# Performance work log

Measured on AMD Instinct MI355X. Metric: run time of the kernel, lower is better.

## Reference

```python
import jax, jax.numpy as jnp
import numpy as np

N = 100000   # nodes
E = 1600000  # edges
F = 128      # input/hidden dim
C = 3        # classes
G = 64       # graphs in batch


def setup_inputs() -> dict:
    key = jax.random.key(0)
    ks = jax.random.split(key, 12)
    s = 1.0 / np.sqrt(F)
    return {
        "x": jax.random.normal(ks[0], (N, F), dtype=jnp.float32),
        "edge_index": jax.random.randint(ks[1], (2, E), 0, N, dtype=jnp.int64),
        "batch": jnp.sort(jax.random.randint(ks[2], (N,), 0, G, dtype=jnp.int64)),
        "W1": jax.random.normal(ks[3], (F, F), dtype=jnp.float32) * s,
        "b1": jnp.zeros((F,), dtype=jnp.float32),
        "W2": jax.random.normal(ks[4], (F, F), dtype=jnp.float32) * s,
        "b2": jnp.zeros((F,), dtype=jnp.float32),
        "W3": jax.random.normal(ks[5], (F, F), dtype=jnp.float32) * s,
        "b3": jnp.zeros((F,), dtype=jnp.float32),
        "Wc": jax.random.normal(ks[6], (F, C), dtype=jnp.float32) * s,
        "bc": jnp.zeros((C,), dtype=jnp.float32),
    }


def reference(x, edge_index, batch, W1, b1, W2, b2, W3, b3, Wc, bc):
    n = x.shape[0]
    src, dst = edge_index[0], edge_index[1]
    # GCN adds self-loops: A_hat = A + I
    loops = jnp.arange(n, dtype=src.dtype)
    src_a = jnp.concatenate([src, loops])
    dst_a = jnp.concatenate([dst, loops])
    # symmetric normalization D^-1/2 (A+I) D^-1/2 (in-degree incl. self-loop)
    deg = jax.ops.segment_sum(jnp.ones_like(dst_a, dtype=x.dtype), dst_a, num_segments=n)
    dis = jnp.where(deg > 0, jax.lax.rsqrt(deg), 0.0)
    norm = dis[src_a] * dis[dst_a]  # [E+N]

    def gcn_conv(h, W, b):
        h = h @ W                                    # [N, F']
        msg = h[src_a] * norm[:, None]               # gather + scale
        agg = jax.ops.segment_sum(msg, dst_a, num_segments=n)  # scatter-add
        return agg + b

    h = jax.nn.relu(gcn_conv(x, W1, b1))   # dropout = identity in eval mode
    h = jax.nn.relu(gcn_conv(h, W2, b2))
    h = jax.nn.relu(gcn_conv(h, W3, b3))

    # global_mean_pool over graph ids
    sums = jax.ops.segment_sum(h, batch, num_segments=G)
    cnt = jax.ops.segment_sum(jnp.ones((n,), dtype=h.dtype), batch, num_segments=G)
    pooled = sums / jnp.maximum(cnt, 1.0)[:, None]
    return pooled @ Wc + bc
```

## Files before the change

### kernel.cpp

```cpp
#include <hip/hip_runtime.h>
#include <cstdint>
#include <cstddef>

#define FDIM 128
#define CHUNK 4096
#define BSHIFT 8
#define BMASK 255
#define MAXB 512

typedef unsigned short ushort_t;
typedef __attribute__((ext_vector_type(8))) short short8;
typedef __attribute__((ext_vector_type(4))) float floatx4;

__device__ inline ushort_t f2bf(float f) {
  unsigned u = __float_as_uint(f);
  u += 0x7fffu + ((u >> 16) & 1u);
  return (ushort_t)(u >> 16);
}
__device__ inline float bf2f(ushort_t h) {
  return __uint_as_float((unsigned)h << 16);
}

__global__ __launch_bounds__(256) void k_histw(const int* __restrict__ dst, int e,
                                               int nb, int* __restrict__ chunkHist,
                                               int nch,
                                               const float* __restrict__ W1,
                                               const float* __restrict__ W2,
                                               const float* __restrict__ W3,
                                               ushort_t* __restrict__ wsw,
                                               int* __restrict__ counter,
                                               float* __restrict__ partials_g,
                                               int g_count) {
  if (blockIdx.x >= (unsigned)nch) {
    int b = blockIdx.x - nch;
    if (b == 3) {
      for (int i = threadIdx.x; i < g_count * FDIM; i += 256) partials_g[i] = 0.f;
      return;
    }
    if (b == 0 && threadIdx.x == 0) *counter = 0;
    const float* W = (b == 0) ? W1 : (b == 1) ? W2 : W3;
    ushort_t* o = wsw + (size_t)b * 16384;
    for (int idx = threadIdx.x; idx < 16384; idx += 256) {
      int j = idx & 7;
      int lane = (idx >> 3) & 63;
      int ct = (idx >> 9) & 7;
      int kc = idx >> 12;
      int k = kc * 32 + (lane >> 4) * 8 + j;
      int col = (lane & 15) * 8 + ct;
      o[idx] = f2bf(W[k * FDIM + col]);
    }
    return;
  }
  __shared__ int h[MAXB];
  int c = blockIdx.x;
  int base = c * CHUNK;
  int end = min(base + CHUNK, e);
  for (int i = threadIdx.x; i < nb; i += 256) h[i] = 0;
  __syncthreads();
  for (int i = base + threadIdx.x; i < end; i += 256)
    atomicAdd(&h[dst[i] >> BSHIFT], 1);
  __syncthreads();
  for (int b = threadIdx.x; b < nb; b += 256)
    chunkHist[(size_t)c * nb + b] = h[b];
}

__global__ __launch_bounds__(512) void k_scan1(const int* __restrict__ chunkHist,
                                               int nchunks, int nb,
                                               int* __restrict__ chunkOff,
                                               int* __restrict__ bucketTotal,
                                               int* __restrict__ bucketBase,
                                               int* __restrict__ counter) {
  __shared__ int sb[512];
  int b = blockIdx.x;
  int t = threadIdx.x;
  int base = 0;
  for (int c0 = 0; c0 < nchunks; c0 += 512) {
    int c = c0 + t;
    int v = (c < nchunks) ? chunkHist[(size_t)c * nb + b] : 0;
    int x = v;
    sb[t] = x;
    __syncthreads();
    for (int off = 1; off < 512; off <<= 1) {
      int y = (t >= off) ? sb[t - off] : 0;
      __syncthreads();
      x += y;
      sb[t] = x;
      __syncthreads();
    }
    if (c < nchunks) chunkOff[(size_t)c * nb + b] = base + x - v;
    int tileTot = sb[511];
    __syncthreads();
    base += tileTot;
  }
  if (t == 0) {
    bucketTotal[b] = base;
    bucketBase[b] = atomicAdd(counter, base);
  }
}

__global__ __launch_bounds__(256) void k_bin(const int* __restrict__ src,
                                             const int* __restrict__ dst, int e, int nb,
                                             const int* __restrict__ chunkHist,
                                             const int* __restrict__ chunkOff,
                                             const int* __restrict__ bucketBase,
                                             unsigned* __restrict__ binned) {
  __shared__ unsigned sortedL[CHUNK];
  __shared__ int gtarget[CHUNK];
  __shared__ int lbase[MAXB], lcur[MAXB], gbase[MAXB];
  __shared__ int stmp[256];
  int c = blockIdx.x;
  int base = c * CHUNK;
  int end = min(base + CHUNK, e);
  for (int i = threadIdx.x; i < nb; i += 256) {
    lbase[i] = chunkHist[(size_t)c * nb + i];
    gbase[i] = bucketBase[i] + chunkOff[(size_t)c * nb + i];
  }
  __syncthreads();
  int carry = 0;
  for (int i0 = 0; i0 < nb; i0 += 256) {
    int i = i0 + threadIdx.x;
    int v = (i < nb) ? lbase[i] : 0;
    int x = v;
    stmp[threadIdx.x] = x;
    __syncthreads();
    for (int off = 1; off < 256; off <<= 1) {
      int y = (threadIdx.x >= off) ? stmp[threadIdx.x - off] : 0;
      __syncthreads();
      x += y;
      stmp[threadIdx.x] = x;
      __syncthreads();
    }
    if (i < nb) lbase[i] = carry + x - v;
    int tileTot = stmp[255];
    __syncthreads();
    carry += tileTot;
  }
  for (int i = threadIdx.x; i < nb; i += 256) lcur[i] = lbase[i];
  __syncthreads();
  for (int i = base + threadIdx.x; i < end; i += 256) {
    int d = dst[i];
    int sv = src[i];
    int b = d >> BSHIFT;
    int slot = atomicAdd(&lcur[b], 1);
    sortedL[slot] = ((unsigned)sv << BSHIFT) | (unsigned)(d & BMASK);
    gtarget[slot] = gbase[b] + (slot - lbase[b]);
  }
  __syncthreads();
  for (int i = threadIdx.x; i < end - base; i += 256)
    binned[gtarget[i]] = sortedL[i];
}

__global__ __launch_bounds__(256) void k_fill2(const unsigned* __restrict__ binned,
                                               const int* __restrict__ bucketBase,
                                               const int* __restrict__ bucketTotal,
                                               int n,
                                               int* __restrict__ rowStart,
                                               int* __restrict__ deg,
                                               float* __restrict__ dis,
                                               unsigned* __restrict__ colPacked) {
  __shared__ int h[256], sb[256], cur[256];
  int b = blockIdx.x;
  int s0 = bucketBase[b], s1 = s0 + bucketTotal[b];
  int nodeBase = b << BSHIFT;
  int t = threadIdx.x;
  h[t] = 0;
  __syncthreads();
  for (int i = s0 + t; i < s1; i += 256) atomicAdd(&h[binned[i] & BMASK], 1);
  __syncthreads();
  int v = h[t];
  int x = v;
  sb[t] = x;
  __syncthreads();
  for (int off = 1; off < 256; off <<= 1) {
    int y = (t >= off) ? sb[t - off] : 0;
    __syncthreads();
    x += y;
    sb[t] = x;
    __syncthreads();
  }
  int start = s0 + x - v;
  cur[t] = start;
  int node = nodeBase + t;
  if (node < n) {
    rowStart[node] = start;
    deg[node] = v;
    dis[node] = rsqrtf((float)(v + 1));
  }
  __syncthreads();
  for (int i = s0 + t; i < s1; i += 256) {
    unsigned en = binned[i];
    int slot = atomicAdd(&cur[en & BMASK], 1);
    colPacked[slot] = en >> BSHIFT;
  }
}

template <int INBF, int EDGW>
__global__ __launch_bounds__(256) void k_mm(const void* __restrict__ Ain,
                                            const ushort_t* __restrict__ Wsw,
                                            ushort_t* __restrict__ O, int n, int mmb,
                                            unsigned* __restrict__ colPacked, int e,
                                            const float* __restrict__ dis) {
  if (EDGW && blockIdx.x >= (unsigned)mmb) {
    int base = (blockIdx.x - mmb) * 2048 + threadIdx.x;
    for (int k = 0; k < 8; ++k) {
      int i = base + k * 256;
      if (i < e) {
        unsigned p = colPacked[i];
        colPacked[i] = p | ((unsigned)f2bf(dis[p]) << 17);
      }
    }
    return;
  }
  __shared__ ushort_t Bs[16384];
  int tid = threadIdx.x;
  for (int q = tid; q < 2048; q += 256)
    ((uint4*)Bs)[q] = ((const uint4*)Wsw)[q];
  __syncthreads();

  int w = tid >> 6;
  int lane = tid & 63;
  int quad = lane >> 4;
  int l15 = lane & 15;
  int rb = blockIdx.x * 128 + w * 32;
  const float* Af = (const float*)Ain;
  const ushort_t* Ab = (const ushort_t*)Ain;

  int row0 = rb + l15;
  int row1 = rb + 16 + l15;
  bool v0 = row0 < n, v1 = row1 < n;

  floatx4 acc[2][8];
#pragma unroll
  for (int rt = 0; rt < 2; ++rt)
#pragma unroll
    for (int ct = 0; ct < 8; ++ct) acc[rt][ct] = floatx4{0.f, 0.f, 0.f, 0.f};

#pragma unroll
  for (int kc = 0; kc < 4; ++kc) {
    int k0 = kc * 32 + quad * 8;
    short8 a0 = short8{0, 0, 0, 0, 0, 0, 0, 0};
    short8 a1 = short8{0, 0, 0, 0, 0, 0, 0, 0};
    if (INBF) {
      if (v0) a0 = *(const short8*)&Ab[(size_t)row0 * FDIM + k0];
      if (v1) a1 = *(const short8*)&Ab[(size_t)row1 * FDIM + k0];
    } else {
      if (v0) {
        float4 f0 = *(const float4*)&Af[(size_t)row0 * FDIM + k0];
        float4 f1 = *(const float4*)&Af[(size_t)row0 * FDIM + k0 + 4];
        a0 = short8{(short)f2bf(f0.x), (short)f2bf(f0.y), (short)f2bf(f0.z),
                    (short)f2bf(f0.w), (short)f2bf(f1.x), (short)f2bf(f1.y),
                    (short)f2bf(f1.z), (short)f2bf(f1.w)};
      }
      if (v1) {
        float4 f0 = *(const float4*)&Af[(size_t)row1 * FDIM + k0];
        float4 f1 = *(const float4*)&Af[(size_t)row1 * FDIM + k0 + 4];
        a1 = short8{(short)f2bf(f0.x), (short)f2bf(f0.y), (short)f2bf(f0.z),
                    (short)f2bf(f0.w), (short)f2bf(f1.x), (short)f2bf(f1.y),
                    (short)f2bf(f1.z), (short)f2bf(f1.w)};
      }
    }
#pragma unroll
    for (int ct = 0; ct < 8; ++ct) {
      short8 bf = *(const short8*)&Bs[((kc * 8 + ct) * 64 + lane) * 8];
      acc[0][ct] = __builtin_amdgcn_mfma_f32_16x16x32_bf16(a0, bf, acc[0][ct], 0, 0, 0);
      acc[1][ct] = __builtin_amdgcn_mfma_f32_16x16x32_bf16(a1, bf, acc[1][ct], 0, 0, 0);
    }
  }

#pragma unroll
  for (int rt = 0; rt < 2; ++rt) {
#pragma unroll
    for (int i = 0; i < 4; ++i) {
      int row = rb + rt * 16 + quad * 4 + i;
      if (row < n) {
        uint4 pk;
        pk.x = (unsigned)f2bf(acc[rt][0][i]) | ((unsigned)f2bf(acc[rt][1][i]) << 16);
        pk.y = (unsigned)f2bf(acc[rt][2][i]) | ((unsigned)f2bf(acc[rt][3][i]) << 16);
        pk.z = (unsigned)f2bf(acc[rt][4][i]) | ((unsigned)f2bf(acc[rt][5][i]) << 16);
        pk.w = (unsigned)f2bf(acc[rt][6][i]) | ((unsigned)f2bf(acc[rt][7][i]) << 16);
        *(uint4*)&O[(size_t)row * FDIM + l15 * 8] = pk;
      }
    }
  }
}

template <int POOL>
__global__ __launch_bounds__(256) void k_agg(const ushort_t* __restrict__ Hin,
                                             ushort_t* __restrict__ Hout,
                                             const int* __restrict__ rowStart,
                                             const int* __restrict__ degE,
                                             const unsigned* __restrict__ colPacked,
                                             const float* __restrict__ dis,
                                             const float* __restrict__ bias, int n,
                                             const int* __restrict__ batch,
                                             float* __restrict__ partials_blk,
                                             float* __restrict__ partials_g) {
  __shared__ float pool_s[POOL ? 4 * FDIM : 4];
  __shared__ int done;
  int tid = threadIdx.x;
  if (POOL) {
    if (tid == 0) done = 0;
    __syncthreads();
  }
  int node = blockIdx.x * 8 + (tid >> 5);
  int lane = tid & 31;
  bool act = node < n;
  if (!POOL && !act) return;
  float a0 = 0.f, a1 = 0.f, a2 = 0.f, a3 = 0.f;
  if (act) {
    const uint2* hin = (const uint2*)Hin;
    float di = dis[node];
    uint2 su = hin[(size_t)node * 32 + lane];
    float ws = di * di;
    a0 = ws * __uint_as_float(su.x << 16);
    a1 = ws * __uint_as_float(su.x & 0xffff0000u);
    a2 = ws * __uint_as_float(su.y << 16);
    a3 = ws * __uint_as_float(su.y & 0xffff0000u);
    int s0 = rowStart[node], cnt = degE[node];
    const unsigned* __restrict__ cp = colPacked + s0;

    int j = 0;
    int main8 = cnt & ~7;
    if (main8) {
      unsigned pv[8];
#pragma unroll
      for (int k = 0; k < 8; ++k) pv[k] = cp[k];
      for (;;) {
        uint2 u[8];
#pragma unroll
        for (int k = 0; k < 8; ++k)
          u[k] = hin[(size_t)(pv[k] & 0x1ffffu) * 32 + lane];
        int jn = j + 8;
        bool more = jn < main8;
        unsigned pn[8];
        if (more) {
#pragma unroll
          for (int k = 0; k < 8; ++k) pn[k] = cp[jn + k];
        }
#pragma unroll
        for (int k = 0; k < 8; ++k) {
          float w = di * __uint_as_float((pv[k] >> 17) << 16);
          a0 += w * __uint_as_float(u[k].x << 16);
          a1 += w * __uint_as_float(u[k].x & 0xffff0000u);
          a2 += w * __uint_as_float(u[k].y << 16);
          a3 += w * __uint_as_float(u[k].y & 0xffff0000u);
        }
        j = jn;
        if (!more) break;
#pragma unroll
        for (int k = 0; k < 8; ++k) pv[k] = pn[k];
      }
    }
    if (j + 4 <= cnt) {
      unsigned pv[4];
#pragma unroll
      for (int k = 0; k < 4; ++k) pv[k] = cp[j + k];
      uint2 u[4];
#pragma unroll
      for (int k = 0; k < 4; ++k)
        u[k] = hin[(size_t)(pv[k] & 0x1ffffu) * 32 + lane];
#pragma unroll
      for (int k = 0; k < 4; ++k) {
        float w = di * __uint_as_float((pv[k] >> 17) << 16);
        a0 += w * __uint_as_float(u[k].x << 16);
        a1 += w * __uint_as_float(u[k].x & 0xffff0000u);
        a2 += w * __uint_as_float(u[k].y << 16);
        a3 += w * __uint_as_float(u[k].y & 0xffff0000u);
      }
      j += 4;
    }
    for (; j < cnt; ++j) {
      unsigned pv = cp[j];
      int sidx = (int)(pv & 0x1ffffu);
      float w = di * __uint_as_float((pv >> 17) << 16);
      uint2 u = hin[(size_t)sidx * 32 + lane];
      a0 += w * __uint_as_float(u.x << 16);
      a1 += w * __uint_as_float(u.x & 0xffff0000u);
      a2 += w * __uint_as_float(u.y << 16);
      a3 += w * __uint_as_float(u.y & 0xffff0000u);
    }
    float4 b = ((const float4*)bias)[lane];
    a0 = fmaxf(a0 + b.x, 0.f);
    a1 = fmaxf(a1 + b.y, 0.f);
    a2 = fmaxf(a2 + b.z, 0.f);
    a3 = fmaxf(a3 + b.w, 0.f);
    if (!POOL) {
      uint2 o;
      o.x = (unsigned)f2bf(a0) | ((unsigned)f2bf(a1) << 16);
      o.y = (unsigned)f2bf(a2) | ((unsigned)f2bf(a3) << 16);
      ((uint2*)Hout)[(size_t)node * 32 + lane] = o;
    }
  }
  if (POOL) {
    int base = blockIdx.x * 8;
    int lastn = min(base + 7, n - 1);
    int g0 = batch[base];
    int sg = (g0 == batch[lastn]) ? g0 : -1;
    int w = tid >> 6;
    int wl = tid & 63;
    int pl = wl ^ 32;
    float p0 = __shfl(a0, pl);
    float p1 = __shfl(a1, pl);
    float p2 = __shfl(a2, pl);
    float p3 = __shfl(a3, pl);
    if (sg >= 0) {
      if (wl < 32) {
        float4 v = {a0 + p0, a1 + p1, a2 + p2, a3 + p3};
        *(float4*)&pool_s[w * FDIM + wl * 4] = v;
      }
    } else {
      if (wl < 32) *(float4*)&pool_s[w * FDIM + wl * 4] = float4{0.f, 0.f, 0.f, 0.f};
      if (act) {
        int gn = batch[node];
        float* pg = &partials_g[(size_t)gn * FDIM + lane * 4];
        atomicAdd(pg + 0, a0);
        atomicAdd(pg + 1, a1);
        atomicAdd(pg + 2, a2);
        atomicAdd(pg + 3, a3);
      }
    }
    __threadfence_block();
    int old = 0;
    if (wl == 0) old = atomicAdd(&done, 1);
    old = __shfl(old, 0);
    if (old == 3) {
      int c = wl * 2;
      float s0 = 0.f, s1 = 0.f;
#pragma unroll
      for (int ww = 0; ww < 4; ++ww) {
        float2 v = *(float2*)&pool_s[ww * FDIM + c];
        s0 += v.x;
        s1 += v.y;
      }
      *(float2*)&partials_blk[(size_t)blockIdx.x * FDIM + c] = float2{s0, s1};
    }
  }
}


__device__ inline int lower_bound_batch(const int* __restrict__ batch, int n, int g) {
  int lo = 0, hi = n;
  while (lo < hi) {
    int mid = (lo + hi) >> 1;
    if (batch[mid] < g) lo = mid + 1;
    else hi = mid;
  }
  return lo;
}

__global__ __launch_bounds__(128) void k_final(const float* __restrict__ partials_blk,
                                               const float* __restrict__ partials_g,
                                               const int* __restrict__ batch, int n,
                                               const float* __restrict__ Wc,
                                               const float* __restrict__ bc,
                                               float* __restrict__ out, int g_count) {
  __shared__ int se[2];
  __shared__ float red[6];
  int t = threadIdx.x;
  int g = blockIdx.x;
  if (t < 2) se[t] = lower_bound_batch(batch, n, g + t);
  __syncthreads();
  int s = se[0], e = se[1];
  float acc = partials_g[(size_t)g * FDIM + t];
  for (int b = (s + 7) >> 3; b * 8 < e; ++b) {
    if (b * 8 + 8 <= e || e >= n)
      acc += partials_blk[(size_t)b * FDIM + t];
  }
  float inv = 1.0f / (float)max(e - s, 1);
  float sv = acc * inv;
#pragma unroll
  for (int c = 0; c < 3; ++c) {
    float v = sv * Wc[t * 3 + c];
#pragma unroll
    for (int off = 1; off < 64; off <<= 1) v += __shfl_xor(v, off);
    if ((t & 63) == 0) red[(t >> 6) * 3 + c] = v;
  }
  __syncthreads();
  if (t < 3) out[g * 3 + t] = red[t] + red[3 + t] + bc[t];
}


extern "C" void kernel_launch(void* const* d_in, const int* in_sizes, int n_in,
                              void* d_out, int out_size, void* d_ws, size_t ws_size,
                              hipStream_t stream) {
  const float* x = (const float*)d_in[0];
  const int* edge = (const int*)d_in[1];
  const int* batch = (const int*)d_in[2];
  const float* W1 = (const float*)d_in[3];
  const float* b1 = (const float*)d_in[4];
  const float* W2 = (const float*)d_in[5];
  const float* b2 = (const float*)d_in[6];
  const float* W3 = (const float*)d_in[7];
  const float* b3 = (const float*)d_in[8];
  const float* Wc = (const float*)d_in[9];
  const float* bc = (const float*)d_in[10];
  float* out = (float*)d_out;

  const int N = in_sizes[0] / FDIM;
  const int E = in_sizes[1] / 2;
  const int G = out_size / 3;
  const int* src = edge;
  const int* dst = edge + E;

  const int NCH = (E + CHUNK - 1) / CHUNK;
  const int NB = (N + (1 << BSHIFT) - 1) >> BSHIFT;

  char* ws = (char*)d_ws;
  size_t off = 0;
  auto carve = [&](size_t bytes) -> void* {
    void* p = ws + off;
    off = (off + bytes + 255) & ~(size_t)255;
    return p;
  };
  int aggb = (N + 7) / 8;
  ushort_t* h0 = (ushort_t*)carve((size_t)N * FDIM * 2);
  ushort_t* h1 = (ushort_t*)carve((size_t)N * FDIM * 2);
  unsigned* colPacked = (unsigned*)carve((size_t)E * 4);
  unsigned* binned = (unsigned*)carve((size_t)E * 4);
  int* chunkHist = (int*)carve((size_t)NCH * NB * 4);
  int* chunkOff = (int*)carve((size_t)NCH * NB * 4);
  int* bucketTotal = (int*)carve((size_t)NB * 4);
  int* bucketBase = (int*)carve((size_t)NB * 4);
  int* counter = (int*)carve(256);
  int* rowStart = (int*)carve((size_t)N * 4);
  int* deg = (int*)carve((size_t)N * 4);
  float* dis = (float*)carve((size_t)N * 4);
  float* partials_g = (float*)carve((size_t)G * FDIM * 4);
  float* partials_blk = (float*)carve((size_t)aggb * FDIM * 4);
  ushort_t* wsw = (ushort_t*)carve((size_t)3 * 16384 * 2);
  (void)n_in;
  (void)ws_size;

  k_histw<<<NCH + 4, 256, 0, stream>>>(dst, E, NB, chunkHist, NCH, W1, W2, W3, wsw,
                                       counter, partials_g, G);
  k_scan1<<<NB, 512, 0, stream>>>(chunkHist, NCH, NB, chunkOff, bucketTotal,
                                  bucketBase, counter);
  k_bin<<<NCH, 256, 0, stream>>>(src, dst, E, NB, chunkHist, chunkOff, bucketBase,
                                 binned);
  k_fill2<<<NB, 256, 0, stream>>>(binned, bucketBase, bucketTotal, N, rowStart, deg,
                                  dis, colPacked);

  int mmb = (N + 127) / 128;
  int ewb = (E + 2047) / 2048;
  k_mm<0, 1><<<mmb + ewb, 256, 0, stream>>>(x, wsw, h0, N, mmb, colPacked, E, dis);
  k_agg<0><<<aggb, 256, 0, stream>>>(h0, h1, rowStart, deg, colPacked, dis, b1, N,
                                     nullptr, nullptr, nullptr);
  k_mm<1, 0><<<mmb, 256, 0, stream>>>(h1, wsw + 16384, h0, N, mmb, nullptr, 0,
                                      nullptr);
  k_agg<0><<<aggb, 256, 0, stream>>>(h0, h1, rowStart, deg, colPacked, dis, b2, N,
                                     nullptr, nullptr, nullptr);
  k_mm<1, 0><<<mmb, 256, 0, stream>>>(h1, wsw + 32768, h0, N, mmb, nullptr, 0,
                                      nullptr);
  k_agg<1><<<aggb, 256, 0, stream>>>(h0, h1, rowStart, deg, colPacked, dis, b3, N,
                                     batch, partials_blk, partials_g);

  k_final<<<G, 128, 0, stream>>>(partials_blk, partials_g, batch, N, Wc, bc, out, G);
}
```

Measured before the change: 434.7 us.

## Fuse first matmul into histogram kernel and drop packed edge weights

Moves the layer-1 matmul (x@W1, converting W1 to bf16 in-block) into the front kernel alongside the dst histogram and W2/W3 swizzle, so it runs concurrently with CSR construction instead of after it. Removes the edge-weight packing pass that embedded bf16 dis into colPacked; aggregation now gathers dis[src] directly per edge, adding an extra scattered 4-byte load per edge in each of three layers. Also widens k_final to 512 threads, splitting the per-graph partial-block reduction across 4 row groups.

```diff
diff --git a/kernel.cpp b/kernel.cpp
--- a/kernel.cpp
+++ b/kernel.cpp
@@ -21,26 +21,41 @@
   return __uint_as_float((unsigned)h << 16);
 }
 
-__global__ __launch_bounds__(256) void k_histw(const int* __restrict__ dst, int e,
-                                               int nb, int* __restrict__ chunkHist,
-                                               int nch,
-                                               const float* __restrict__ W1,
-                                               const float* __restrict__ W2,
-                                               const float* __restrict__ W3,
-                                               ushort_t* __restrict__ wsw,
-                                               int* __restrict__ counter,
-                                               float* __restrict__ partials_g,
-                                               int g_count) {
-  if (blockIdx.x >= (unsigned)nch) {
-    int b = blockIdx.x - nch;
-    if (b == 3) {
-      for (int i = threadIdx.x; i < g_count * FDIM; i += 256) partials_g[i] = 0.f;
+__global__ __launch_bounds__(256) void k_front(
+    const float* __restrict__ x, const float* __restrict__ W1,
+    const float* __restrict__ W2, const float* __restrict__ W3,
+    ushort_t* __restrict__ h0, int n, int mmb,
+    const int* __restrict__ dst, int e, int nb,
+    int* __restrict__ chunkHist, int nch,
+    ushort_t* __restrict__ wsw, int* __restrict__ counter,
+    float* __restrict__ partials_g, int g_count) {
+  __shared__ ushort_t Bs[16384];
+  int tid = threadIdx.x;
+  int bid = blockIdx.x;
+  if (bid >= mmb) {
+    int r = bid - mmb;
+    if (r < nch) {
+      int* h = (int*)Bs;
+      int base = r * CHUNK;
+      int end = min(base + CHUNK, e);
+      for (int i = tid; i < nb; i += 256) h[i] = 0;
+      __syncthreads();
+      for (int i = base + tid; i < end; i += 256)
+        atomicAdd(&h[dst[i] >> BSHIFT], 1);
+      __syncthreads();
+      for (int b = tid; b < nb; b += 256)
+        chunkHist[(size_t)r * nb + b] = h[b];
       return;
     }
-    if (b == 0 && threadIdx.x == 0) *counter = 0;
-    const float* W = (b == 0) ? W1 : (b == 1) ? W2 : W3;
+    int b = r - nch;
+    if (b == 2) {
+      for (int i = tid; i < g_count * FDIM; i += 256) partials_g[i] = 0.f;
+      return;
+    }
+    if (b == 0 && tid == 0) *counter = 0;
+    const float* W = (b == 0) ? W2 : W3;
     ushort_t* o = wsw + (size_t)b * 16384;
-    for (int idx = threadIdx.x; idx < 16384; idx += 256) {
+    for (int idx = tid; idx < 16384; idx += 256) {
       int j = idx & 7;
       int lane = (idx >> 3) & 63;
       int ct = (idx >> 9) & 7;
@@ -51,17 +66,85 @@
     }
     return;
   }
-  __shared__ int h[MAXB];
-  int c = blockIdx.x;
-  int base = c * CHUNK;
-  int end = min(base + CHUNK, e);
-  for (int i = threadIdx.x; i < nb; i += 256) h[i] = 0;
-  __syncthreads();
-  for (int i = base + threadIdx.x; i < end; i += 256)
-    atomicAdd(&h[dst[i] >> BSHIFT], 1);
-  __syncthreads();
-  for (int b = threadIdx.x; b < nb; b += 256)
-    chunkHist[(size_t)c * nb + b] = h[b];
+  for (int q = tid; q < 2048; q += 256) {
+    int lane = q & 63;
+    int ct = (q >> 6) & 7;
+    int kc = q >> 9;
+    int col = (lane & 15) * 8 + ct;
+    int kb = kc * 32 + (lane >> 4) * 8;
+    unsigned t0 = f2bf(W1[(kb + 0) * FDIM + col]);
+    unsigned t1 = f2bf(W1[(kb + 1) * FDIM + col]);
+    unsigned t2 = f2bf(W1[(kb + 2) * FDIM + col]);
+    unsigned t3 = f2bf(W1[(kb + 3) * FDIM + col]);
+    unsigned t4 = f2bf(W1[(kb + 4) * FDIM + col]);
+    unsigned t5 = f2bf(W1[(kb + 5) * FDIM + col]);
+    unsigned t6 = f2bf(W1[(kb + 6) * FDIM + col]);
+    unsigned t7 = f2bf(W1[(kb + 7) * FDIM + col]);
+    uint4 pk;
+    pk.x = t0 | (t1 << 16);
+    pk.y = t2 | (t3 << 16);
+    pk.z = t4 | (t5 << 16);
+    pk.w = t6 | (t7 << 16);
+    ((uint4*)Bs)[q] = pk;
+  }
+  __syncthreads();
+
+  int w = tid >> 6;
+  int lane = tid & 63;
+  int quad = lane >> 4;
+  int l15 = lane & 15;
+  int rb = bid * 128 + w * 32;
+  int row0 = rb + l15;
+  int row1 = rb + 16 + l15;
+  bool v0 = row0 < n, v1 = row1 < n;
+
+  floatx4 acc[2][8];
+#pragma unroll
+  for (int rt = 0; rt < 2; ++rt)
+#pragma unroll
+    for (int ct = 0; ct < 8; ++ct) acc[rt][ct] = floatx4{0.f, 0.f, 0.f, 0.f};
+
+#pragma unroll
+  for (int kc = 0; kc < 4; ++kc) {
+    int k0 = kc * 32 + quad * 8;
+    short8 a0 = short8{0, 0, 0, 0, 0, 0, 0, 0};
+    short8 a1 = short8{0, 0, 0, 0, 0, 0, 0, 0};
+    if (v0) {
+      float4 f0 = *(const float4*)&x[(size_t)row0 * FDIM + k0];
+      float4 f1 = *(const float4*)&x[(size_t)row0 * FDIM + k0 + 4];
+      a0 = short8{(short)f2bf(f0.x), (short)f2bf(f0.y), (short)f2bf(f0.z),
+                  (short)f2bf(f0.w), (short)f2bf(f1.x), (short)f2bf(f1.y),
+                  (short)f2bf(f1.z), (short)f2bf(f1.w)};
+    }
+    if (v1) {
+      float4 f0 = *(const float4*)&x[(size_t)row1 * FDIM + k0];
+      float4 f1 = *(const float4*)&x[(size_t)row1 * FDIM + k0 + 4];
+      a1 = short8{(short)f2bf(f0.x), (short)f2bf(f0.y), (short)f2bf(f0.z),
+                  (short)f2bf(f0.w), (short)f2bf(f1.x), (short)f2bf(f1.y),
+                  (short)f2bf(f1.z), (short)f2bf(f1.w)};
+    }
+#pragma unroll
+    for (int ct = 0; ct < 8; ++ct) {
+      short8 bf = *(const short8*)&Bs[((kc * 8 + ct) * 64 + lane) * 8];
+      acc[0][ct] = __builtin_amdgcn_mfma_f32_16x16x32_bf16(a0, bf, acc[0][ct], 0, 0, 0);
+      acc[1][ct] = __builtin_amdgcn_mfma_f32_16x16x32_bf16(a1, bf, acc[1][ct], 0, 0, 0);
+    }
+  }
+#pragma unroll
+  for (int rt = 0; rt < 2; ++rt) {
+#pragma unroll
+    for (int i = 0; i < 4; ++i) {
+      int row = rb + rt * 16 + quad * 4 + i;
+      if (row < n) {
+        uint4 pk;
+        pk.x = (unsigned)f2bf(acc[rt][0][i]) | ((unsigned)f2bf(acc[rt][1][i]) << 16);
+        pk.y = (unsigned)f2bf(acc[rt][2][i]) | ((unsigned)f2bf(acc[rt][3][i]) << 16);
+        pk.z = (unsigned)f2bf(acc[rt][4][i]) | ((unsigned)f2bf(acc[rt][5][i]) << 16);
+        pk.w = (unsigned)f2bf(acc[rt][6][i]) | ((unsigned)f2bf(acc[rt][7][i]) << 16);
+        *(uint4*)&h0[(size_t)row * FDIM + l15 * 8] = pk;
+      }
+    }
+  }
 }
 
 __global__ __launch_bounds__(512) void k_scan1(const int* __restrict__ chunkHist,
@@ -194,23 +277,9 @@
   }
 }
 
-template <int INBF, int EDGW>
-__global__ __launch_bounds__(256) void k_mm(const void* __restrict__ Ain,
+__global__ __launch_bounds__(256) void k_mm(const ushort_t* __restrict__ Ain,
                                             const ushort_t* __restrict__ Wsw,
-                                            ushort_t* __restrict__ O, int n, int mmb,
-                                            unsigned* __restrict__ colPacked, int e,
-                                            const float* __restrict__ dis) {
-  if (EDGW && blockIdx.x >= (unsigned)mmb) {
-    int base = (blockIdx.x - mmb) * 2048 + threadIdx.x;
-    for (int k = 0; k < 8; ++k) {
-      int i = base + k * 256;
-      if (i < e) {
-        unsigned p = colPacked[i];
-        colPacked[i] = p | ((unsigned)f2bf(dis[p]) << 17);
-      }
-    }
-    return;
-  }
+                                            ushort_t* __restrict__ O, int n) {
   __shared__ ushort_t Bs[16384];
   int tid = threadIdx.x;
   for (int q = tid; q < 2048; q += 256)
@@ -222,8 +291,6 @@
   int quad = lane >> 4;
   int l15 = lane & 15;
   int rb = blockIdx.x * 128 + w * 32;
-  const float* Af = (const float*)Ain;
-  const ushort_t* Ab = (const ushort_t*)Ain;
 
   int row0 = rb + l15;
   int row1 = rb + 16 + l15;
@@ -240,25 +307,8 @@
     int k0 = kc * 32 + quad * 8;
     short8 a0 = short8{0, 0, 0, 0, 0, 0, 0, 0};
     short8 a1 = short8{0, 0, 0, 0, 0, 0, 0, 0};
-    if (INBF) {
-      if (v0) a0 = *(const short8*)&Ab[(size_t)row0 * FDIM + k0];
-      if (v1) a1 = *(const short8*)&Ab[(size_t)row1 * FDIM + k0];
-    } else {
-      if (v0) {
-        float4 f0 = *(const float4*)&Af[(size_t)row0 * FDIM + k0];
-        float4 f1 = *(const float4*)&Af[(size_t)row0 * FDIM + k0 + 4];
-        a0 = short8{(short)f2bf(f0.x), (short)f2bf(f0.y), (short)f2bf(f0.z),
-                    (short)f2bf(f0.w), (short)f2bf(f1.x), (short)f2bf(f1.y),
-                    (short)f2bf(f1.z), (short)f2bf(f1.w)};
-      }
-      if (v1) {
-        float4 f0 = *(const float4*)&Af[(size_t)row1 * FDIM + k0];
-        float4 f1 = *(const float4*)&Af[(size_t)row1 * FDIM + k0 + 4];
-        a1 = short8{(short)f2bf(f0.x), (short)f2bf(f0.y), (short)f2bf(f0.z),
-                    (short)f2bf(f0.w), (short)f2bf(f1.x), (short)f2bf(f1.y),
-                    (short)f2bf(f1.z), (short)f2bf(f1.w)};
-      }
-    }
+    if (v0) a0 = *(const short8*)&Ain[(size_t)row0 * FDIM + k0];
+    if (v1) a1 = *(const short8*)&Ain[(size_t)row1 * FDIM + k0];
 #pragma unroll
     for (int ct = 0; ct < 8; ++ct) {
       short8 bf = *(const short8*)&Bs[((kc * 8 + ct) * 64 + lane) * 8];
@@ -326,10 +376,13 @@
 #pragma unroll
       for (int k = 0; k < 8; ++k) pv[k] = cp[k];
       for (;;) {
+        float dv[8];
         uint2 u[8];
 #pragma unroll
-        for (int k = 0; k < 8; ++k)
-          u[k] = hin[(size_t)(pv[k] & 0x1ffffu) * 32 + lane];
+        for (int k = 0; k < 8; ++k) {
+          dv[k] = dis[(int)pv[k]];
+          u[k] = hin[(size_t)pv[k] * 32 + lane];
+        }
         int jn = j + 8;
         bool more = jn < main8;
         unsigned pn[8];
@@ -339,7 +392,7 @@
         }
 #pragma unroll
         for (int k = 0; k < 8; ++k) {
-          float w = di * __uint_as_float((pv[k] >> 17) << 16);
+          float w = di * dv[k];
           a0 += w * __uint_as_float(u[k].x << 16);
           a1 += w * __uint_as_float(u[k].x & 0xffff0000u);
           a2 += w * __uint_as_float(u[k].y << 16);
@@ -355,13 +408,16 @@
       unsigned pv[4];
 #pragma unroll
       for (int k = 0; k < 4; ++k) pv[k] = cp[j + k];
+      float dv[4];
       uint2 u[4];
 #pragma unroll
-      for (int k = 0; k < 4; ++k)
-        u[k] = hin[(size_t)(pv[k] & 0x1ffffu) * 32 + lane];
-#pragma unroll
       for (int k = 0; k < 4; ++k) {
-        float w = di * __uint_as_float((pv[k] >> 17) << 16);
+        dv[k] = dis[(int)pv[k]];
+        u[k] = hin[(size_t)pv[k] * 32 + lane];
+      }
+#pragma unroll
+      for (int k = 0; k < 4; ++k) {
+        float w = di * dv[k];
         a0 += w * __uint_as_float(u[k].x << 16);
         a1 += w * __uint_as_float(u[k].x & 0xffff0000u);
         a2 += w * __uint_as_float(u[k].y << 16);
@@ -371,9 +427,8 @@
     }
     for (; j < cnt; ++j) {
       unsigned pv = cp[j];
-      int sidx = (int)(pv & 0x1ffffu);
-      float w = di * __uint_as_float((pv >> 17) << 16);
-      uint2 u = hin[(size_t)sidx * 32 + lane];
+      float w = di * dis[(int)pv];
+      uint2 u = hin[(size_t)pv * 32 + lane];
       a0 += w * __uint_as_float(u.x << 16);
       a1 += w * __uint_as_float(u.x & 0xffff0000u);
       a2 += w * __uint_as_float(u.y << 16);
@@ -448,32 +503,39 @@
   return lo;
 }
 
-__global__ __launch_bounds__(128) void k_final(const float* __restrict__ partials_blk,
+__global__ __launch_bounds__(512) void k_final(const float* __restrict__ partials_blk,
                                                const float* __restrict__ partials_g,
                                                const int* __restrict__ batch, int n,
                                                const float* __restrict__ Wc,
                                                const float* __restrict__ bc,
                                                float* __restrict__ out, int g_count) {
+  __shared__ float red2[4][FDIM];
   __shared__ int se[2];
   __shared__ float red[6];
   int t = threadIdx.x;
+  int f = t & 127;
+  int r = t >> 7;
   int g = blockIdx.x;
   if (t < 2) se[t] = lower_bound_batch(batch, n, g + t);
   __syncthreads();
   int s = se[0], e = se[1];
-  float acc = partials_g[(size_t)g * FDIM + t];
-  for (int b = (s + 7) >> 3; b * 8 < e; ++b) {
+  float acc = (r == 0) ? partials_g[(size_t)g * FDIM + f] : 0.f;
+  for (int b = ((s + 7) >> 3) + r; b * 8 < e; b += 4) {
     if (b * 8 + 8 <= e || e >= n)
-      acc += partials_blk[(size_t)b * FDIM + t];
-  }
-  float inv = 1.0f / (float)max(e - s, 1);
-  float sv = acc * inv;
-#pragma unroll
-  for (int c = 0; c < 3; ++c) {
-    float v = sv * Wc[t * 3 + c];
-#pragma unroll
-    for (int off = 1; off < 64; off <<= 1) v += __shfl_xor(v, off);
-    if ((t & 63) == 0) red[(t >> 6) * 3 + c] = v;
+      acc += partials_blk[(size_t)b * FDIM + f];
+  }
+  red2[r][f] = acc;
+  __syncthreads();
+  if (t < FDIM) {
+    float sv = (red2[0][t] + red2[1][t] + red2[2][t] + red2[3][t]) /
+               (float)max(e - s, 1);
+#pragma unroll
+    for (int c = 0; c < 3; ++c) {
+      float v = sv * Wc[t * 3 + c];
+#pragma unroll
+      for (int off = 1; off < 64; off <<= 1) v += __shfl_xor(v, off);
+      if ((t & 63) == 0) red[(t >> 6) * 3 + c] = v;
+    }
   }
   __syncthreads();
   if (t < 3) out[g * 3 + t] = red[t] + red[3 + t] + bc[t];
@@ -527,12 +589,14 @@
   float* dis = (float*)carve((size_t)N * 4);
   float* partials_g = (float*)carve((size_t)G * FDIM * 4);
   float* partials_blk = (float*)carve((size_t)aggb * FDIM * 4);
-  ushort_t* wsw = (ushort_t*)carve((size_t)3 * 16384 * 2);
+  ushort_t* wsw = (ushort_t*)carve((size_t)2 * 16384 * 2);
   (void)n_in;
   (void)ws_size;
 
-  k_histw<<<NCH + 4, 256, 0, stream>>>(dst, E, NB, chunkHist, NCH, W1, W2, W3, wsw,
-                                       counter, partials_g, G);
+  int mmb = (N + 127) / 128;
+  k_front<<<mmb + NCH + 3, 256, 0, stream>>>(x, W1, W2, W3, h0, N, mmb, dst, E, NB,
+                                             chunkHist, NCH, wsw, counter,
+                                             partials_g, G);
   k_scan1<<<NB, 512, 0, stream>>>(chunkHist, NCH, NB, chunkOff, bucketTotal,
                                   bucketBase, counter);
   k_bin<<<NCH, 256, 0, stream>>>(src, dst, E, NB, chunkHist, chunkOff, bucketBase,
@@ -540,19 +604,14 @@
   k_fill2<<<NB, 256, 0, stream>>>(binned, bucketBase, bucketTotal, N, rowStart, deg,
                                   dis, colPacked);
 
-  int mmb = (N + 127) / 128;
-  int ewb = (E + 2047) / 2048;
-  k_mm<0, 1><<<mmb + ewb, 256, 0, stream>>>(x, wsw, h0, N, mmb, colPacked, E, dis);
   k_agg<0><<<aggb, 256, 0, stream>>>(h0, h1, rowStart, deg, colPacked, dis, b1, N,
                                      nullptr, nullptr, nullptr);
-  k_mm<1, 0><<<mmb, 256, 0, stream>>>(h1, wsw + 16384, h0, N, mmb, nullptr, 0,
-                                      nullptr);
+  k_mm<<<mmb, 256, 0, stream>>>(h1, wsw, h0, N);
   k_agg<0><<<aggb, 256, 0, stream>>>(h0, h1, rowStart, deg, colPacked, dis, b2, N,
                                      nullptr, nullptr, nullptr);
-  k_mm<1, 0><<<mmb, 256, 0, stream>>>(h1, wsw + 32768, h0, N, mmb, nullptr, 0,
-                                      nullptr);
+  k_mm<<<mmb, 256, 0, stream>>>(h1, wsw + 16384, h0, N);
   k_agg<1><<<aggb, 256, 0, stream>>>(h0, h1, rowStart, deg, colPacked, dis, b3, N,
                                      batch, partials_blk, partials_g);
 
-  k_final<<<G, 128, 0, stream>>>(partials_blk, partials_g, batch, N, Wc, bc, out, G);
-}
+  k_final<<<G, 512, 0, stream>>>(partials_blk, partials_g, batch, N, Wc, bc, out, G);
+}
```

Result: faster. 419.0 us (-3.6%).
